# Kernel tuning notes

Measured on AMD Instinct MI355X. Metric: run time of the kernel, lower is better.

Reference implementation:

```python
import jax, jax.numpy as jnp
import numpy as np

B, T, D, H, L, C = 512, 512, 128, 16, 5, 2


def setup_inputs() -> dict:
    key = jax.random.key(0)
    ks = jax.random.split(key, 12)
    x = jax.random.normal(ks[0], (B, T, D), dtype=jnp.float32)
    # pack_padded_sequence requires descending lengths; force max length == T
    lengths = jnp.sort(jax.random.randint(ks[1], (B,), 1, T + 1))[::-1]
    lengths = lengths.at[0].set(T)
    s = 0.25  # ~ 1/sqrt(H) init scale
    W_ih0 = jax.random.normal(ks[2], (3 * H, D), dtype=jnp.float32) * s
    W_ihr = jax.random.normal(ks[3], (L - 1, 3 * H, H), dtype=jnp.float32) * s
    W_hh = jax.random.normal(ks[4], (L, 3 * H, H), dtype=jnp.float32) * s
    b_ih = jax.random.normal(ks[5], (L, 3 * H), dtype=jnp.float32) * s
    b_hh = jax.random.normal(ks[6], (L, 3 * H), dtype=jnp.float32) * s
    W_fc = jax.random.normal(ks[7], (C, H), dtype=jnp.float32) * s
    b_fc = jax.random.normal(ks[8], (C,), dtype=jnp.float32) * s
    return {"x": x, "lengths": lengths, "W_ih0": W_ih0, "W_ihr": W_ihr,
            "W_hh": W_hh, "b_ih": b_ih, "b_hh": b_hh, "W_fc": W_fc, "b_fc": b_fc}


def _gru_layer(seq, Wih, Whh, bih, bhh):
    # seq: [T, B, Din] -> outputs [T, B, H]. PyTorch GRU gate math.
    xg = jnp.einsum('tbd,gd->tbg', seq, Wih) + bih  # precompute input projections

    def step(h, xg_t):
        hg = h @ Whh.T + bhh
        xr, xz, xn = jnp.split(xg_t, 3, axis=-1)
        hr, hz, hn = jnp.split(hg, 3, axis=-1)
        r = jax.nn.sigmoid(xr + hr)
        z = jax.nn.sigmoid(xz + hz)
        n = jnp.tanh(xn + r * hn)
        h_new = (1.0 - z) * n + z * h
        return h_new, h_new

    h0 = jnp.zeros((seq.shape[1], Whh.shape[1]), seq.dtype)
    _, ys = jax.lax.scan(step, h0, xg)
    return ys


def reference(x, lengths, W_ih0, W_ihr, W_hh, b_ih, b_hh, W_fc, b_fc):
    seq = jnp.transpose(x, (1, 0, 2))  # [T, B, D]
    seq = _gru_layer(seq, W_ih0, W_hh[0], b_ih[0], b_hh[0])
    for l in range(L - 1):  # dropout(0.5) between layers: eval mode (identity)
        seq = _gru_layer(seq, W_ihr[l], W_hh[l + 1], b_ih[l + 1], b_hh[l + 1])
    last = seq[T - 1]  # [B, H] == padded output[:, -1, :]
    # pad_packed_sequence zero-pads: rows with length < T are zero at t = T-1
    last = jnp.where((lengths == T)[:, None], last, 0.0)
    return last @ W_fc.T + b_fc
```

## Files before the change

### kernel.cpp

```cpp
#include <hip/hip_runtime.h>


constexpr int kB = 512, kT = 512, kD = 128, kH = 16, kL = 5, kC = 2, kG = 48;
constexpr int kChunk = 16, kNC = kT / kChunk, kThreads = 448;
constexpr int kPhases = kNC + 2 * (kL - 1);
constexpr int kYW = 64;
constexpr float kLog2e = 1.4426950408889634f;

typedef unsigned uint2v __attribute__((ext_vector_type(2)));

__device__ __forceinline__ float rl(float v, int lane) {
    return __int_as_float(__builtin_amdgcn_readlane(__float_as_int(v), lane));
}

__device__ __forceinline__ float fexp2(float x) {
#if __has_builtin(__builtin_amdgcn_exp2f)
    return __builtin_amdgcn_exp2f(x);
#else
    return exp2f(x);
#endif
}

#if __has_builtin(__builtin_amdgcn_permlane32_swap) && __has_builtin(__builtin_amdgcn_permlane16_swap)
#define HAVE_PERMLANE 1
__device__ __forceinline__ float xor32(float v, bool d) {
    uint2v r = __builtin_amdgcn_permlane32_swap(__float_as_uint(v), __float_as_uint(v), false, false);
    return __uint_as_float(d ? r[0] : r[1]);
}
__device__ __forceinline__ float xor16(float v, bool d) {
    uint2v r = __builtin_amdgcn_permlane16_swap(__float_as_uint(v), __float_as_uint(v), false, false);
    return __uint_as_float(d ? r[0] : r[1]);
}
#else
#define HAVE_PERMLANE 0
__device__ __forceinline__ float bperm_xor(float v, int xmask) {
    int lane = threadIdx.x & 63;
    return __int_as_float(__builtin_amdgcn_ds_bpermute((lane ^ xmask) * 4, __float_as_int(v)));
}
__device__ __forceinline__ float xor32(float v, bool) { return bperm_xor(v, 32); }
__device__ __forceinline__ float xor16(float v, bool) { return bperm_xor(v, 16); }
#endif

__device__ __forceinline__ float gru_step(float h, float xg,
                                          const float (&wreg)[kH], float bh,
                                          bool d32, bool d16) {
    float a0 = bh, a1 = 0.f, a2 = 0.f, a3 = 0.f;
    float a4 = 0.f, a5 = 0.f, a6 = 0.f, a7 = 0.f;
    #pragma unroll
    for (int k = 0; k < 2; ++k) {
        a0 = fmaf(rl(h, k),      wreg[k],      a0);
        a1 = fmaf(rl(h, k + 2),  wreg[k + 2],  a1);
        a2 = fmaf(rl(h, k + 4),  wreg[k + 4],  a2);
        a3 = fmaf(rl(h, k + 6),  wreg[k + 6],  a3);
        a4 = fmaf(rl(h, k + 8),  wreg[k + 8],  a4);
        a5 = fmaf(rl(h, k + 10), wreg[k + 10], a5);
        a6 = fmaf(rl(h, k + 12), wreg[k + 12], a6);
        a7 = fmaf(rl(h, k + 14), wreg[k + 14], a7);
    }
    float xnb = xor32(xg, d32);
    float hg = (((a0 + a1) + (a2 + a3)) + ((a4 + a5) + (a6 + a7)));
    float hnb = xor32(hg, d32);
    float s = xg + hg;
    float sig = __builtin_amdgcn_rcpf(1.0f + fexp2(-s));
    float zb = xor16(sig, d16);
    float narg = fmaf(sig, hnb, xnb);
    float nv = fmaf(-2.0f, __builtin_amdgcn_rcpf(fexp2(narg) + 1.0f), 1.0f);
    return fmaf(zb, h - nv, nv);
}

template<bool WY>
__device__ __forceinline__ float scan_lds(float h, const float* __restrict__ xb,
                                          float (*__restrict__ yout)[kYW],
                                          const float (&wreg)[kH], float bh,
                                          int lane, bool d32, bool d16)
{
    float xgc = xb[0];
    #pragma unroll
    for (int tt = 0; tt < kChunk; ++tt) {
        float xgn = (tt + 1 < kChunk) ? xb[(tt + 1) * kG] : 0.0f;
        h = gru_step(h, xgc, wreg, bh, d32, d16);
        if (WY) yout[tt][lane] = h;
        xgc = xgn;
    }
    return h;
}

template<bool SCAN, int PREP>
__device__ __forceinline__ float phase_w0(
    float h, float (&xgr)[kChunk], const float* __restrict__ gsrc,
    float (*__restrict__ yout)[kYW],
    const float (&wreg)[kH], float bh, int lane, bool d32, bool d16)
{
    #pragma unroll
    for (int tt = 0; tt < kChunk; ++tt) {
        if (SCAN) {
            h = gru_step(h, xgr[tt], wreg, bh, d32, d16);
            yout[tt][lane] = h;
        }
        if (PREP == 1) xgr[tt] = gsrc[(size_t)tt * kG];
    }
    return h;
}

__device__ __forceinline__ void prep_layer(
    const float (*__restrict__ yp)[kYW], float* __restrict__ xb,
    const float (&wih)[kH], float bi, int g)
{
    #pragma unroll
    for (int tt = 0; tt < kChunk; ++tt) {
        const float4* y4 = (const float4*)&yp[tt][0];
        float4 y0 = y4[0], y1 = y4[1], y2 = y4[2], y3 = y4[3];
        float p0 = bi, p1 = 0.f, p2 = 0.f, p3 = 0.f;
        p0 = fmaf(y0.x, wih[0],  p0); p0 = fmaf(y0.y, wih[1],  p0);
        p0 = fmaf(y0.z, wih[2],  p0); p0 = fmaf(y0.w, wih[3],  p0);
        p1 = fmaf(y1.x, wih[4],  p1); p1 = fmaf(y1.y, wih[5],  p1);
        p1 = fmaf(y1.z, wih[6],  p1); p1 = fmaf(y1.w, wih[7],  p1);
        p2 = fmaf(y2.x, wih[8],  p2); p2 = fmaf(y2.y, wih[9],  p2);
        p2 = fmaf(y2.z, wih[10], p2); p2 = fmaf(y2.w, wih[11], p2);
        p3 = fmaf(y3.x, wih[12], p3); p3 = fmaf(y3.y, wih[13], p3);
        p3 = fmaf(y3.z, wih[14], p3); p3 = fmaf(y3.w, wih[15], p3);
        xb[tt * kG + g] = (p0 + p1) + (p2 + p3);
    }
}

extern "C" __global__ void __launch_bounds__(256, 1)
proj0(const float* __restrict__ x, const int* __restrict__ len,
      const float* __restrict__ Wih0, const float* __restrict__ bih,
      float* __restrict__ xg0, int qmax)
{
    const int blk = blockIdx.x;
    const int b = blk >> 4, s = blk & 15;
    if (b >= qmax || len[b] != kT) return;
    const int tid = threadIdx.x;
    #pragma unroll
    for (int i = 0; i < 6; ++i) {
        int item = tid + 256 * i;
        int t = item / kG, g = item - t * kG;
        const float4* xr = (const float4*)(x + ((size_t)b * kT + s * 32 + t) * kD);
        const float4* wr = (const float4*)(Wih0 + (size_t)g * kD);
        float a0 = 0.f, a1 = 0.f, a2 = 0.f, a3 = 0.f;
        #pragma unroll 8
        for (int k = 0; k < kD / 4; ++k) {
            float4 xv = xr[k], wv = wr[k];
            a0 = fmaf(xv.x, wv.x, a0);
            a1 = fmaf(xv.y, wv.y, a1);
            a2 = fmaf(xv.z, wv.z, a2);
            a3 = fmaf(xv.w, wv.w, a3);
        }
        float scg = (g < 32) ? kLog2e : 2.0f * kLog2e;
        xg0[((size_t)b * kT + s * 32 + t) * kG + g] =
            scg * (bih[g] + ((a0 + a1) + (a2 + a3)));
    }
}

__device__ void proj_chunk_wave0(const float* __restrict__ x,
                                 const float* __restrict__ Wih0,
                                 const float* __restrict__ bih,
                                 int b, int c, int lane, float (*__restrict__ XW0)[kG])
{
    for (int i = 0; i < kChunk * kG / 64; ++i) {
        int item = lane + 64 * i;
        int t = item / kG, g = item - t * kG;
        const float4* xr = (const float4*)(x + ((size_t)b * kT + c * kChunk + t) * kD);
        const float4* wr = (const float4*)(Wih0 + (size_t)g * kD);
        float a0 = 0.f, a1 = 0.f, a2 = 0.f, a3 = 0.f;
        #pragma unroll 8
        for (int k = 0; k < kD / 4; ++k) {
            float4 xv = xr[k], wv = wr[k];
            a0 = fmaf(xv.x, wv.x, a0);
            a1 = fmaf(xv.y, wv.y, a1);
            a2 = fmaf(xv.z, wv.z, a2);
            a3 = fmaf(xv.w, wv.w, a3);
        }
        float scg = (g < 32) ? kLog2e : 2.0f * kLog2e;
        XW0[t][g] = scg * (bih[g] + ((a0 + a1) + (a2 + a3)));
    }
}

__device__ __forceinline__ void barrier_lgkm() {
    asm volatile("s_waitcnt lgkmcnt(0)" ::: "memory");
    __builtin_amdgcn_s_barrier();
}

extern "C" __global__ void __launch_bounds__(kThreads, 1)
gru_pipe8(const float* __restrict__ x, const int* __restrict__ len,
          const float* __restrict__ Wih0, const float* __restrict__ Wihr,
          const float* __restrict__ Whh, const float* __restrict__ bih,
          const float* __restrict__ bhh, const float* __restrict__ Wfc,
          const float* __restrict__ bfc, const float* __restrict__ xg0,
          float* __restrict__ out, int qmax)
{
    const int b = blockIdx.x;
    const int tid = threadIdx.x;

    if (len[b] != kT) {
        if (tid < kC) out[b * kC + tid] = bfc[tid];
        return;
    }

    __shared__ float Yr[kL - 1][2][kChunk][kYW];
    __shared__ float XB[kL - 1][2][kChunk][kG];
    __shared__ float XW0[kChunk][kG];
    __shared__ float hfin[kH];

    const int wid = tid >> 6, lane = tid & 63;
    const int g = (lane < kG) ? lane : (kG - 1);
    const bool fast = (b < qmax);
    const float* xgb = xg0 + (size_t)b * kT * kG + g;
    const float sc = (g < 32) ? kLog2e : 2.0f * kLog2e;

    const int lay = (wid == 0) ? 0 : (wid == 1) ? 4 : (wid == 2) ? 1
                  : (wid == 4) ? 2 : (wid == 6) ? 3 : -1;
    const bool isPrep = (lay < 0);
    const int pA = (wid == 3) ? 1 : 3;
    const int pB = pA + 1;

#if HAVE_PERMLANE
    uint2v pr32 = __builtin_amdgcn_permlane32_swap((unsigned)lane, (unsigned)lane, false, false);
    uint2v pr16 = __builtin_amdgcn_permlane16_swap((unsigned)lane, (unsigned)lane, false, false);
    const bool d32 = (pr32[0] == (unsigned)(lane ^ 32));
    const bool d16 = (pr16[0] == (unsigned)(lane ^ 16));
#else
    const bool d32 = false, d16 = false;
#endif

    float wreg[kH], wihA[kH], wihB[kH];
    float bh = 0.f, biA = 0.f, biB = 0.f, h = 0.f;
    if (!isPrep) {
        const float* wrow = Whh + (size_t)(lay * kG + g) * kH;
        #pragma unroll
        for (int k = 0; k < kH; ++k) { wreg[k] = wrow[k] * sc; wihA[k] = 0.f; wihB[k] = 0.f; }
        bh = bhh[lay * kG + g] * sc;
    } else {
        const float* wa = Wihr + (size_t)((pA - 1) * kG + g) * kH;
        const float* wb = Wihr + (size_t)((pB - 1) * kG + g) * kH;
        #pragma unroll
        for (int k = 0; k < kH; ++k) { wihA[k] = wa[k] * sc; wihB[k] = wb[k] * sc; wreg[k] = 0.f; }
        biA = bih[pA * kG + g] * sc;
        biB = bih[pB * kG + g] * sc;
    }

    float xgr[kChunk];
    if (wid == 0) {
        if (fast) {
            #pragma unroll
            for (int tt = 0; tt < kChunk; ++tt) xgr[tt] = xgb[(size_t)tt * kG];
        } else {
            proj_chunk_wave0(x, Wih0, bih, b, 0, lane, XW0);
            asm volatile("s_waitcnt lgkmcnt(0)" ::: "memory");
            #pragma unroll
            for (int tt = 0; tt < kChunk; ++tt) xgr[tt] = XW0[tt][g];
        }
    }

    for (int p = 0; p < kPhases; ++p) {
        if (wid == 0) {
            const int c = p;
            if (c < kNC) {
                float (*yo)[kYW] = Yr[0][c & 1];
                if (fast) {
                    const float* gsrc = xgb + (size_t)(c + 1) * kChunk * kG;
                    if (c + 1 < kNC)
                        h = phase_w0<true, 1>(h, xgr, gsrc, yo, wreg, bh, lane, d32, d16);
                    else
                        h = phase_w0<true, 0>(h, xgr, nullptr, yo, wreg, bh, lane, d32, d16);
                } else {
                    h = phase_w0<true, 0>(h, xgr, nullptr, yo, wreg, bh, lane, d32, d16);
                    if (c + 1 < kNC) {
                        proj_chunk_wave0(x, Wih0, bih, b, c + 1, lane, XW0);
                        asm volatile("s_waitcnt lgkmcnt(0)" ::: "memory");
                        #pragma unroll
                        for (int tt = 0; tt < kChunk; ++tt) xgr[tt] = XW0[tt][g];
                    }
                }
            }
        } else if (!isPrep) {
            const int c = p - 2 * lay;
            if (c >= 0 && c < kNC) {
                const float* xb = &XB[lay - 1][c & 1][0][0] + g;
                if (lay < kL - 1)
                    h = scan_lds<true>(h, xb, Yr[lay][c & 1], wreg, bh, lane, d32, d16);
                else
                    h = scan_lds<false>(h, xb, Yr[0][0], wreg, bh, lane, d32, d16);
            }
        } else {
            const int nA = p + 1 - 2 * pA;
            if (nA >= 0 && nA < kNC)
                prep_layer(Yr[pA - 1][nA & 1], &XB[pA - 1][nA & 1][0][0], wihA, biA, g);
            const int nB = p + 1 - 2 * pB;
            if (nB >= 0 && nB < kNC)
                prep_layer(Yr[pB - 1][nB & 1], &XB[pB - 1][nB & 1][0][0], wihB, biB, g);
        }
        barrier_lgkm();
    }

    if (wid == 1 && lane < kH) hfin[lane] = h;
    __syncthreads();

    if (tid < kC) {
        float acc = bfc[tid];
        #pragma unroll
        for (int j = 0; j < kH; ++j)
            acc = fmaf(hfin[j], Wfc[tid * kH + j], acc);
        out[b * kC + tid] = acc;
    }
}

extern "C" void kernel_launch(void* const* d_in, const int* in_sizes, int n_in,
                              void* d_out, int out_size, void* d_ws, size_t ws_size,
                              hipStream_t stream) {
    const float* x    = (const float*)d_in[0];
    const int*   len  = (const int*)d_in[1];
    const float* Wih0 = (const float*)d_in[2];
    const float* Wihr = (const float*)d_in[3];
    const float* Whh  = (const float*)d_in[4];
    const float* bih  = (const float*)d_in[5];
    const float* bhh  = (const float*)d_in[6];
    const float* Wfc  = (const float*)d_in[7];
    const float* bfc  = (const float*)d_in[8];
    float* outp = (float*)d_out;
    float* xg0  = (float*)d_ws;

    size_t per_row = (size_t)kT * kG * sizeof(float);
    int qmax = (int)((ws_size / per_row) < (size_t)kB ? (ws_size / per_row) : (size_t)kB);

    hipLaunchKernelGGL(proj0, dim3(kB * 16), dim3(256), 0, stream,
                       x, len, Wih0, bih, xg0, qmax);
    hipLaunchKernelGGL(gru_pipe8, dim3(kB), dim3(kThreads), 0, stream,
                       x, len, Wih0, Wihr, Whh, bih, bhh, Wfc, bfc, xg0, outp, qmax);
}
```

Measured before the change: 182.1 us.

## Fuse input projection into recurrent scan waves and shorten the layer pipeline

```diff
diff --git a/kernel.cpp b/kernel.cpp
--- a/kernel.cpp
+++ b/kernel.cpp
@@ -2,8 +2,8 @@
 
 
 constexpr int kB = 512, kT = 512, kD = 128, kH = 16, kL = 5, kC = 2, kG = 48;
-constexpr int kChunk = 16, kNC = kT / kChunk, kThreads = 448;
-constexpr int kPhases = kNC + 2 * (kL - 1);
+constexpr int kChunk = 16, kNC = kT / kChunk, kThreads = 320;
+constexpr int kPhases = kNC + kL - 1;
 constexpr int kYW = 64;
 constexpr float kLog2e = 1.4426950408889634f;
 
@@ -64,23 +64,47 @@
     float sig = __builtin_amdgcn_rcpf(1.0f + fexp2(-s));
     float zb = xor16(sig, d16);
     float narg = fmaf(sig, hnb, xnb);
-    float nv = fmaf(-2.0f, __builtin_amdgcn_rcpf(fexp2(narg) + 1.0f), 1.0f);
-    return fmaf(zb, h - nv, nv);
+    float R = __builtin_amdgcn_rcpf(fexp2(narg) + 1.0f);
+    float u = 1.0f - zb;
+    float K = fmaf(zb, h, u);
+    float m = -2.0f * u;
+    return fmaf(m, R, K);
+}
+
+__device__ __forceinline__ float dot16(const float4& y0, const float4& y1,
+                                       const float4& y2, const float4& y3,
+                                       const float (&w)[kH], float bias) {
+    float p0 = bias, p1 = 0.f, p2 = 0.f, p3 = 0.f;
+    p0 = fmaf(y0.x, w[0],  p0); p0 = fmaf(y0.y, w[1],  p0);
+    p0 = fmaf(y0.z, w[2],  p0); p0 = fmaf(y0.w, w[3],  p0);
+    p1 = fmaf(y1.x, w[4],  p1); p1 = fmaf(y1.y, w[5],  p1);
+    p1 = fmaf(y1.z, w[6],  p1); p1 = fmaf(y1.w, w[7],  p1);
+    p2 = fmaf(y2.x, w[8],  p2); p2 = fmaf(y2.y, w[9],  p2);
+    p2 = fmaf(y2.z, w[10], p2); p2 = fmaf(y2.w, w[11], p2);
+    p3 = fmaf(y3.x, w[12], p3); p3 = fmaf(y3.y, w[13], p3);
+    p3 = fmaf(y3.z, w[14], p3); p3 = fmaf(y3.w, w[15], p3);
+    return (p0 + p1) + (p2 + p3);
 }
 
 template<bool WY>
-__device__ __forceinline__ float scan_lds(float h, const float* __restrict__ xb,
-                                          float (*__restrict__ yout)[kYW],
-                                          const float (&wreg)[kH], float bh,
-                                          int lane, bool d32, bool d16)
-{
-    float xgc = xb[0];
+__device__ __forceinline__ float scan_prep(
+    float h, const float (*__restrict__ yprev)[kYW], float (*__restrict__ yout)[kYW],
+    const float (&wreg)[kH], float bh, const float (&wih)[kH], float bi,
+    int lane, bool d32, bool d16)
+{
+    const float4* y4 = (const float4*)&yprev[0][0];
+    float4 ra0 = y4[0], ra1 = y4[1], ra2 = y4[2], ra3 = y4[3];
+    float xg = dot16(ra0, ra1, ra2, ra3, wih, bi);
     #pragma unroll
     for (int tt = 0; tt < kChunk; ++tt) {
-        float xgn = (tt + 1 < kChunk) ? xb[(tt + 1) * kG] : 0.0f;
-        h = gru_step(h, xgc, wreg, bh, d32, d16);
+        float4 rb0, rb1, rb2, rb3;
+        if (tt + 1 < kChunk) {
+            const float4* yn = (const float4*)&yprev[tt + 1][0];
+            rb0 = yn[0]; rb1 = yn[1]; rb2 = yn[2]; rb3 = yn[3];
+        }
+        h = gru_step(h, xg, wreg, bh, d32, d16);
         if (WY) yout[tt][lane] = h;
-        xgc = xgn;
+        if (tt + 1 < kChunk) xg = dot16(rb0, rb1, rb2, rb3, wih, bi);
     }
     return h;
 }
@@ -100,27 +124,6 @@
         if (PREP == 1) xgr[tt] = gsrc[(size_t)tt * kG];
     }
     return h;
-}
-
-__device__ __forceinline__ void prep_layer(
-    const float (*__restrict__ yp)[kYW], float* __restrict__ xb,
-    const float (&wih)[kH], float bi, int g)
-{
-    #pragma unroll
-    for (int tt = 0; tt < kChunk; ++tt) {
-        const float4* y4 = (const float4*)&yp[tt][0];
-        float4 y0 = y4[0], y1 = y4[1], y2 = y4[2], y3 = y4[3];
-        float p0 = bi, p1 = 0.f, p2 = 0.f, p3 = 0.f;
-        p0 = fmaf(y0.x, wih[0],  p0); p0 = fmaf(y0.y, wih[1],  p0);
-        p0 = fmaf(y0.z, wih[2],  p0); p0 = fmaf(y0.w, wih[3],  p0);
-        p1 = fmaf(y1.x, wih[4],  p1); p1 = fmaf(y1.y, wih[5],  p1);
-        p1 = fmaf(y1.z, wih[6],  p1); p1 = fmaf(y1.w, wih[7],  p1);
-        p2 = fmaf(y2.x, wih[8],  p2); p2 = fmaf(y2.y, wih[9],  p2);
-        p2 = fmaf(y2.z, wih[10], p2); p2 = fmaf(y2.w, wih[11], p2);
-        p3 = fmaf(y3.x, wih[12], p3); p3 = fmaf(y3.y, wih[13], p3);
-        p3 = fmaf(y3.z, wih[14], p3); p3 = fmaf(y3.w, wih[15], p3);
-        xb[tt * kG + g] = (p0 + p1) + (p2 + p3);
-    }
 }
 
 extern "C" __global__ void __launch_bounds__(256, 1)
@@ -183,7 +186,7 @@
 }
 
 extern "C" __global__ void __launch_bounds__(kThreads, 1)
-gru_pipe8(const float* __restrict__ x, const int* __restrict__ len,
+gru_pipe9(const float* __restrict__ x, const int* __restrict__ len,
           const float* __restrict__ Wih0, const float* __restrict__ Wihr,
           const float* __restrict__ Whh, const float* __restrict__ bih,
           const float* __restrict__ bhh, const float* __restrict__ Wfc,
@@ -199,7 +202,6 @@
     }
 
     __shared__ float Yr[kL - 1][2][kChunk][kYW];
-    __shared__ float XB[kL - 1][2][kChunk][kG];
     __shared__ float XW0[kChunk][kG];
     __shared__ float hfin[kH];
 
@@ -208,12 +210,6 @@
     const bool fast = (b < qmax);
     const float* xgb = xg0 + (size_t)b * kT * kG + g;
     const float sc = (g < 32) ? kLog2e : 2.0f * kLog2e;
-
-    const int lay = (wid == 0) ? 0 : (wid == 1) ? 4 : (wid == 2) ? 1
-                  : (wid == 4) ? 2 : (wid == 6) ? 3 : -1;
-    const bool isPrep = (lay < 0);
-    const int pA = (wid == 3) ? 1 : 3;
-    const int pB = pA + 1;
 
 #if HAVE_PERMLANE
     uint2v pr32 = __builtin_amdgcn_permlane32_swap((unsigned)lane, (unsigned)lane, false, false);
@@ -224,20 +220,22 @@
     const bool d32 = false, d16 = false;
 #endif
 
-    float wreg[kH], wihA[kH], wihB[kH];
-    float bh = 0.f, biA = 0.f, biB = 0.f, h = 0.f;
-    if (!isPrep) {
-        const float* wrow = Whh + (size_t)(lay * kG + g) * kH;
+    float wreg[kH], wih[kH];
+    float bh, bi = 0.f, h = 0.f;
+    {
+        const float* wrow = Whh + (size_t)(wid * kG + g) * kH;
         #pragma unroll
-        for (int k = 0; k < kH; ++k) { wreg[k] = wrow[k] * sc; wihA[k] = 0.f; wihB[k] = 0.f; }
-        bh = bhh[lay * kG + g] * sc;
-    } else {
-        const float* wa = Wihr + (size_t)((pA - 1) * kG + g) * kH;
-        const float* wb = Wihr + (size_t)((pB - 1) * kG + g) * kH;
-        #pragma unroll
-        for (int k = 0; k < kH; ++k) { wihA[k] = wa[k] * sc; wihB[k] = wb[k] * sc; wreg[k] = 0.f; }
-        biA = bih[pA * kG + g] * sc;
-        biB = bih[pB * kG + g] * sc;
+        for (int k = 0; k < kH; ++k) wreg[k] = wrow[k] * sc;
+        bh = bhh[wid * kG + g] * sc;
+        if (wid > 0) {
+            const float* wr2 = Wihr + (size_t)((wid - 1) * kG + g) * kH;
+            #pragma unroll
+            for (int k = 0; k < kH; ++k) wih[k] = wr2[k] * sc;
+            bi = bih[wid * kG + g] * sc;
+        } else {
+            #pragma unroll
+            for (int k = 0; k < kH; ++k) wih[k] = 0.f;
+        }
     }
 
     float xgr[kChunk];
@@ -274,27 +272,20 @@
                     }
                 }
             }
-        } else if (!isPrep) {
-            const int c = p - 2 * lay;
+        } else {
+            const int c = p - wid;
             if (c >= 0 && c < kNC) {
-                const float* xb = &XB[lay - 1][c & 1][0][0] + g;
-                if (lay < kL - 1)
-                    h = scan_lds<true>(h, xb, Yr[lay][c & 1], wreg, bh, lane, d32, d16);
+                const float (*yp)[kYW] = Yr[wid - 1][c & 1];
+                if (wid < kL - 1)
+                    h = scan_prep<true>(h, yp, Yr[wid][c & 1], wreg, bh, wih, bi, lane, d32, d16);
                 else
-                    h = scan_lds<false>(h, xb, Yr[0][0], wreg, bh, lane, d32, d16);
+                    h = scan_prep<false>(h, yp, Yr[0][0], wreg, bh, wih, bi, lane, d32, d16);
             }
-        } else {
-            const int nA = p + 1 - 2 * pA;
-            if (nA >= 0 && nA < kNC)
-                prep_layer(Yr[pA - 1][nA & 1], &XB[pA - 1][nA & 1][0][0], wihA, biA, g);
-            const int nB = p + 1 - 2 * pB;
-            if (nB >= 0 && nB < kNC)
-                prep_layer(Yr[pB - 1][nB & 1], &XB[pB - 1][nB & 1][0][0], wihB, biB, g);
         }
         barrier_lgkm();
     }
 
-    if (wid == 1 && lane < kH) hfin[lane] = h;
+    if (wid == kL - 1 && lane < kH) hfin[lane] = h;
     __syncthreads();
 
     if (tid < kC) {
@@ -326,6 +317,6 @@
 
     hipLaunchKernelGGL(proj0, dim3(kB * 16), dim3(256), 0, stream,
                        x, len, Wih0, bih, xg0, qmax);
-    hipLaunchKernelGGL(gru_pipe8, dim3(kB), dim3(kThreads), 0, stream,
+    hipLaunchKernelGGL(gru_pipe9, dim3(kB), dim3(kThreads), 0, stream,
                        x, len, Wih0, Wihr, Whh, bih, bhh, Wfc, bfc, xg0, outp, qmax);
 }
```

New measurement: 179.1 us. Within noise of the previous version (-1.6%).
